# Kernel optimization log

Measured on AMD Instinct MI355X. Metric: run time of the kernel, lower is better.

## Reference

```python
import jax, jax.numpy as jnp
import numpy as np
from jax import lax

N, C, H, W = 32, 256, 32, 32
E, K, MLP = 8, 2, 4
CAP = 1.25
HID = MLP * C
LN_EPS = 1e-6


def setup_inputs() -> dict:
    key = jax.random.key(0)
    ks = jax.random.split(key, 12)
    s = 0.02
    return {
        "input": jax.random.normal(ks[0], (N, C, H, W), jnp.float32),
        "dw_kernel": jax.random.normal(ks[1], (C, 1, 7, 7), jnp.float32) * s,
        "dw_bias": jnp.zeros((C,), jnp.float32),
        "ln_gamma": jnp.ones((C,), jnp.float32),
        "ln_beta": jnp.zeros((C,), jnp.float32),
        "router_w": jax.random.normal(ks[2], (C, E), jnp.float32) * s,
        "w1": jax.random.normal(ks[3], (E, C, HID), jnp.float32) * s,
        "b1": jnp.zeros((E, HID), jnp.float32),
        "w2": jax.random.normal(ks[4], (E, HID, C), jnp.float32) * s,
        "b2": jnp.zeros((E, C), jnp.float32),
        "layer_scale": jnp.full((C, 1, 1), 1e-6, jnp.float32),
    }


def reference(input, dw_kernel, dw_bias, ln_gamma, ln_beta, router_w,
              w1, b1, w2, b2, layer_scale):
    # depthwise 7x7 conv (groups = C), NCHW
    x = lax.conv_general_dilated(
        input, dw_kernel, window_strides=(1, 1), padding=[(3, 3), (3, 3)],
        dimension_numbers=("NCHW", "OIHW", "NCHW"), feature_group_count=C)
    x = x + dw_bias[None, :, None, None]
    x = jnp.transpose(x, (0, 2, 3, 1))  # NHWC
    # LayerNorm over channels
    mu = jnp.mean(x, axis=-1, keepdims=True)
    var = jnp.mean(jnp.square(x - mu), axis=-1, keepdims=True)
    x = (x - mu) * lax.rsqrt(var + LN_EPS) * ln_gamma + ln_beta

    T = N * H * W
    x_flat = x.reshape(T, C)

    # router (eval mode of NoisyTopKRouter: no noise)
    logits = x_flat @ router_w                      # [T, E]
    top_logits, topi = lax.top_k(logits, K)          # [T, K]
    weights = jax.nn.softmax(top_logits, axis=-1)    # [T, K]
    priority = weights[:, 0]
    order = jnp.argsort(-priority)                   # descending priority

    # build K*T candidates, stably sorted by expert id
    token_idx = jnp.tile(order, K)                           # order.repeat(K)
    expert_id = topi[order].T.reshape(-1)
    gate_w = weights[order].T.reshape(-1)
    perm = jnp.argsort(expert_id)                            # stable
    token_idx, expert_id, gate_w = token_idx[perm], expert_id[perm], gate_w[perm]

    # capacity truncation
    Be = int(K * T * CAP / E + 0.5)
    counts = jnp.bincount(expert_id, length=E)
    starts = jnp.cumsum(counts) - counts
    pos = jnp.arange(K * T) - starts[expert_id]
    keep = pos < Be
    slot = jnp.where(keep, expert_id * Be + pos, E * Be)     # dump slot for drops

    # dispatch to capacity buffers [E, Be, C]
    buf = jnp.zeros((E * Be + 1, C), x_flat.dtype).at[slot].set(x_flat[token_idx])
    buf = buf[:E * Be].reshape(E, Be, C)

    # grouped expert MLP: Linear -> GELU(exact) -> Linear
    h = jax.nn.gelu(jnp.einsum("ebc,ech->ebh", buf, w1) + b1[:, None, :],
                    approximate=False)
    y = jnp.einsum("ebh,ehc->ebc", h, w2) + b2[:, None, :]

    # combine: gather back, gate-scale (zero for dropped), scatter-add
    y_pad = jnp.concatenate([y.reshape(E * Be, C),
                             jnp.zeros((1, C), y.dtype)], axis=0)
    contrib = y_pad[slot] * (gate_w * keep.astype(gate_w.dtype))[:, None]
    out = jnp.zeros((T, C), x_flat.dtype).at[token_idx].add(contrib)

    out = out.reshape(N, H, W, C).transpose(0, 3, 1, 2)      # NCHW
    # stochastic_depth_prob = 0 -> identity
    return input + layer_scale[None] * out
```

## Files before the change

kernel.cpp:

```cpp
#include <hip/hip_runtime.h>
#include <math.h>

#define TOK 32768
#define CH  256
#define HIDN 1024
#define NE  8
#define BE  10240
#define CNT_STRIDE 64

typedef __attribute__((ext_vector_type(8))) short bf16x8;
typedef __attribute__((ext_vector_type(4))) float f32x4;
typedef __attribute__((ext_vector_type(2))) long long2v;

__device__ __forceinline__ unsigned short f2bf(float f) {
    unsigned u = __builtin_bit_cast(unsigned, f);
    unsigned r = 0x7FFFu + ((u >> 16) & 1u);
    return (unsigned short)((u + r) >> 16);
}
__device__ __forceinline__ float bf2f(unsigned short u) {
    return __builtin_bit_cast(float, (unsigned)u << 16);
}
__device__ __forceinline__ unsigned pk8_lo(float a, float b, unsigned old) {
    return (unsigned)__builtin_amdgcn_cvt_pk_fp8_f32(a, b, (int)old, false);
}
__device__ __forceinline__ unsigned pk8_hi(float a, float b, unsigned old) {
    return (unsigned)__builtin_amdgcn_cvt_pk_fp8_f32(a, b, (int)old, true);
}
__device__ __forceinline__ f32x4 mfma8(long a, long b, f32x4 c) {
    return __builtin_amdgcn_mfma_f32_16x16x32_fp8_fp8(a, b, c, 0, 0, 0);
}

typedef __attribute__((address_space(3))) void lds_t;
typedef const __attribute__((address_space(1))) void gm_t;
#define GL16(gp, lp) __builtin_amdgcn_global_load_lds((gm_t*)(gp), (lds_t*)(lp), 16, 0, 0)

__global__ void k_init(int* cnt) { cnt[threadIdx.x] = 0; }

__global__ __launch_bounds__(256) void k_conv(const float* __restrict__ in,
                                              const float* __restrict__ kern,
                                              const float* __restrict__ bias,
                                              unsigned char* __restrict__ xc8) {
    __shared__ float img[1024];
    __shared__ float kwl[49];
    int t = threadIdx.x;
    int bid = blockIdx.x;
    int c = bid & 255;

    GL16(in + (size_t)bid * 1024 + t * 4, (char*)img + t * 16);
    if (t < 49) kwl[t] = kern[c * 49 + t];
    __syncthreads();

    int x0 = (t & 7) * 4, y = t >> 3;
    float b0 = bias[c];
    float acc[4] = {b0, b0, b0, b0};
#pragma unroll
    for (int jr = 0; jr < 7; ++jr) {
        int yy = y + jr - 3;
        if ((unsigned)yy < 32u) {
            float row[10];
#pragma unroll
            for (int k = 0; k < 10; ++k) {
                int xx = x0 - 3 + k;
                row[k] = ((unsigned)xx < 32u) ? img[yy * 32 + xx] : 0.f;
            }
#pragma unroll
            for (int kx = 0; kx < 7; ++kx) {
                float kv = kwl[jr * 7 + kx];
#pragma unroll
                for (int o = 0; o < 4; ++o) acc[o] = fmaf(row[o + kx], kv, acc[o]);
            }
        }
    }
    unsigned u = pk8_lo(acc[0], acc[1], 0u);
    u = pk8_hi(acc[2], acc[3], u);
    *(unsigned*)(xc8 + (size_t)bid * 1024 + y * 32 + x0) = u;
}

__global__ __launch_bounds__(512) void k_lnr(const unsigned char* __restrict__ xc8,
                                             const float* __restrict__ gamma,
                                             const float* __restrict__ beta,
                                             const float* __restrict__ rw,
                                             unsigned* __restrict__ xf8,
                                             int* __restrict__ e01,
                                             float2* __restrict__ gates) {
    __shared__ float acc[32][260];
    int t = threadIdx.x;
    int n = blockIdx.x >> 5, y = blockIdx.x & 31;
    int x4 = t & 7, ch = t >> 3;

#pragma unroll
    for (int i = 0; i < 4; ++i) {
        int c = i * 64 + ch;
        unsigned word = *(const unsigned*)(xc8 + ((size_t)(n * 256 + c)) * 1024 + y * 32 + x4 * 4);
        acc[x4 * 4 + 0][c] = __builtin_amdgcn_cvt_f32_fp8((int)word, 0);
        acc[x4 * 4 + 1][c] = __builtin_amdgcn_cvt_f32_fp8((int)word, 1);
        acc[x4 * 4 + 2][c] = __builtin_amdgcn_cvt_f32_fp8((int)word, 2);
        acc[x4 * 4 + 3][c] = __builtin_amdgcn_cvt_f32_fp8((int)word, 3);
    }
    __syncthreads();

    int lane = t & 63, w = t >> 6;
    float4 g4 = ((const float4*)gamma)[lane];
    float4 b4 = ((const float4*)beta)[lane];
    int c0 = lane * 4;
    float4 rwv[8];
#pragma unroll
    for (int j = 0; j < 4; ++j) {
        rwv[j * 2]     = *(const float4*)(rw + (size_t)(c0 + j) * 8);
        rwv[j * 2 + 1] = *(const float4*)(rw + (size_t)(c0 + j) * 8 + 4);
    }

#pragma unroll
    for (int k = 0; k < 4; ++k) {
        int tl = w * 4 + k;
        float4 v = *(const float4*)&acc[tl][lane * 4];
        float s = v.x + v.y + v.z + v.w;
        float q = v.x * v.x + v.y * v.y + v.z * v.z + v.w * v.w;
#pragma unroll
        for (int m = 1; m < 64; m <<= 1) { s += __shfl_xor(s, m); q += __shfl_xor(q, m); }
        float mean = s * (1.0f / 256.0f);
        float var  = q * (1.0f / 256.0f) - mean * mean;
        float rstd = rsqrtf(var + 1e-6f);

        float xn[4];
        xn[0] = (v.x - mean) * rstd * g4.x + b4.x;
        xn[1] = (v.y - mean) * rstd * g4.y + b4.y;
        xn[2] = (v.z - mean) * rstd * g4.z + b4.z;
        xn[3] = (v.w - mean) * rstd * g4.w + b4.w;

        unsigned px = pk8_lo(xn[0], xn[1], 0u);
        px = pk8_hi(xn[2], xn[3], px);
        int tok = n * 1024 + y * 32 + tl;
        xf8[tok * 64 + lane] = px;

        float p[8];
#pragma unroll
        for (int e = 0; e < 8; ++e) p[e] = 0.f;
#pragma unroll
        for (int j = 0; j < 4; ++j) {
            float xv = xn[j];
            const float* r0 = (const float*)&rwv[j * 2];
#pragma unroll
            for (int e = 0; e < 8; ++e) p[e] += xv * r0[e];
        }
#pragma unroll
        for (int m = 1; m < 64; m <<= 1) {
#pragma unroll
            for (int e = 0; e < 8; ++e) p[e] += __shfl_xor(p[e], m);
        }
        if (lane == 0) {
            int e0 = 0; float l0 = p[0];
#pragma unroll
            for (int e = 1; e < 8; ++e) if (p[e] > l0) { l0 = p[e]; e0 = e; }
            int e1 = -1; float l1 = -3.4e38f;
#pragma unroll
            for (int e = 0; e < 8; ++e) if (e != e0 && p[e] > l1) { l1 = p[e]; e1 = e; }
            float tt = expf(l1 - l0);
            float w0 = 1.0f / (1.0f + tt);
            e01[tok] = e0 | (e1 << 8);
            gates[tok] = make_float2(w0, 1.0f - w0);
        }
    }
}

__global__ __launch_bounds__(256) void k_assign(const int* __restrict__ e01,
                                                int* __restrict__ cnt,
                                                int* __restrict__ row_token,
                                                int2* __restrict__ slots) {
    __shared__ int lcnt[8];
    __shared__ int base[8];
    int t = threadIdx.x;
    if (t < 8) lcnt[t] = 0;
    __syncthreads();
    int tok = blockIdx.x * 256 + t;
    int ee = e01[tok];
    int e0 = ee & 255, e1 = (ee >> 8) & 255;
    int lp0 = atomicAdd(&lcnt[e0], 1);
    int lp1 = atomicAdd(&lcnt[e1], 1);
    __syncthreads();
    if (t < 8) base[t] = atomicAdd(cnt + t * CNT_STRIDE, lcnt[t]);
    __syncthreads();
    int pos0 = base[e0] + lp0;
    int pos1 = base[e1] + lp1;
    int slot0 = (pos0 < BE) ? e0 * BE + pos0 : -1;
    int slot1 = (pos1 < BE) ? e1 * BE + pos1 : -1;
    if (slot0 >= 0) row_token[slot0] = tok;
    if (slot1 >= 0) row_token[slot1] = tok;
    slots[tok] = make_int2(slot0, slot1);
}

__global__ __launch_bounds__(256) void k_pack_w1(const float* __restrict__ w1,
                                                 unsigned char* __restrict__ w1p) {
    int s = blockIdx.x * 256 + threadIdx.x;
    int l = s & 63, tile = s >> 6;
    int kp = tile & 3, h = (tile >> 2) & 1, hc = (tile >> 3) & 31, e = tile >> 8;
    int l15 = l & 15, l4 = l >> 4;
    int hid = hc * 32 + h * 16 + l15;
    int ch0 = kp * 64 + l4 * 8;
    const float* s0 = w1 + ((size_t)e * 256 + ch0) * 1024 + hid;
    float v[8], u[8];
#pragma unroll
    for (int b = 0; b < 8; ++b) { v[b] = s0[b * 1024]; u[b] = s0[(b + 32) * 1024]; }
    uint4 o;
    o.x = pk8_hi(v[2], v[3], pk8_lo(v[0], v[1], 0u));
    o.y = pk8_hi(v[6], v[7], pk8_lo(v[4], v[5], 0u));
    o.z = pk8_hi(u[2], u[3], pk8_lo(u[0], u[1], 0u));
    o.w = pk8_hi(u[6], u[7], pk8_lo(u[4], u[5], 0u));
    *(uint4*)(w1p + (size_t)tile * 1024 + l * 16) = o;
}

__global__ __launch_bounds__(256) void k_pack_w2(const float* __restrict__ w2,
                                                 unsigned char* __restrict__ w2p) {
    int s = blockIdx.x * 256 + threadIdx.x;
    int l = s & 63, tile = s >> 6;
    int np = tile & 7, hc = (tile >> 3) & 31, e = tile >> 8;
    int l15 = l & 15, l4 = l >> 4;
    float v[8], u[8];
#pragma unroll
    for (int b = 0; b < 8; ++b) {
        int hidl = ((b >> 2) & 1) * 16 + l4 * 4 + (b & 3);
        const float* s0 = w2 + ((size_t)e * 1024 + hc * 32 + hidl) * 256 + np * 32 + l15;
        v[b] = s0[0];
        u[b] = s0[16];
    }
    uint4 o;
    o.x = pk8_hi(v[2], v[3], pk8_lo(v[0], v[1], 0u));
    o.y = pk8_hi(v[6], v[7], pk8_lo(v[4], v[5], 0u));
    o.z = pk8_hi(u[2], u[3], pk8_lo(u[0], u[1], 0u));
    o.w = pk8_hi(u[6], u[7], pk8_lo(u[4], u[5], 0u));
    *(uint4*)(w2p + (size_t)tile * 1024 + l * 16) = o;
}

__global__ __launch_bounds__(256, 3) void k_mlp(const unsigned char* __restrict__ xf8,
                                                const unsigned char* __restrict__ w1p,
                                                const unsigned char* __restrict__ w2p,
                                                const float* __restrict__ b1,
                                                const float* __restrict__ b2,
                                                const int* __restrict__ cnt,
                                                const int* __restrict__ row_token,
                                                unsigned short* __restrict__ Y) {
    int bid = blockIdx.x;
    int e = bid & 7;
    int row0 = (bid >> 3) * 64;
    int nrows = min(cnt[e * CNT_STRIDE], BE);
    if (row0 >= nrows) return;

    __shared__ char smem[45056];
    char* const W1S0 = smem;
    char* const W1S1 = smem + 8192;
    char* const W2S0 = smem + 16384;
    char* const W2S1 = smem + 24576;
    char* const W2S2 = smem + 32768;
    char* const b1lds = smem + 40960;

    int t = threadIdx.x;
    int w = t >> 6, lane = t & 63;
    int l15 = lane & 15, l4 = lane >> 4;

    const unsigned char* w1e = w1p + (size_t)e * 262144;
    const unsigned char* w2e = w2p + (size_t)e * 262144;

    int ri = row0 + w * 16 + l15;
    int tok0 = (ri < nrows) ? row_token[e * BE + ri] : 0;
    long xr[8];
#pragma unroll
    for (int ks = 0; ks < 8; ++ks)
        xr[ks] = *(const long*)(xf8 + (size_t)tok0 * 256 + ks * 32 + l4 * 8);

    GL16((const char*)(b1 + e * HIDN) + t * 16, b1lds + t * 16);
    GL16(w1e + t * 16, W1S0 + t * 16);
    GL16(w1e + 4096 + t * 16, W1S0 + 4096 + t * 16);
    GL16(w2e + t * 16, W2S0 + t * 16);
    GL16(w2e + 4096 + t * 16, W2S0 + 4096 + t * 16);
    __builtin_amdgcn_sched_barrier(0);
    asm volatile("s_waitcnt vmcnt(2)" ::: "memory");
    __builtin_amdgcn_s_barrier();
    __builtin_amdgcn_sched_barrier(0);

    f32x4 yacc[16];
#pragma unroll
    for (int nc = 0; nc < 16; ++nc) yacc[nc] = f32x4{0.f, 0.f, 0.f, 0.f};

    long hfA = 0, hfB = 0;

    auto STEP = [&](const char* w1c, const char* w2r, char* w1f_, char* w2f_,
                    const unsigned char* g1, const unsigned char* g2,
                    bool doStage, bool doB, long hin, long& hout,
                    int b1off, bool last) {
        if (doStage) {
            GL16(g1 + t * 16, w1f_ + t * 16);
            GL16(g1 + 4096 + t * 16, w1f_ + 4096 + t * 16);
            GL16(g2 + t * 16, w2f_ + t * 16);
            GL16(g2 + 4096 + t * 16, w2f_ + 4096 + t * 16);
        }
        long w1fr[2][8];
#pragma unroll
        for (int h = 0; h < 2; ++h)
#pragma unroll
            for (int kp = 0; kp < 4; ++kp) {
                long2v q = *(const long2v*)(w1c + (h * 4 + kp) * 1024 + lane * 16);
                w1fr[h][kp * 2] = q.x;
                w1fr[h][kp * 2 + 1] = q.y;
            }
        f32x4 ha0 = f32x4{0.f, 0.f, 0.f, 0.f};
        f32x4 ha1 = f32x4{0.f, 0.f, 0.f, 0.f};
#pragma unroll
        for (int ks = 0; ks < 8; ++ks) {
            ha0 = mfma8(w1fr[0][ks], xr[ks], ha0);
            ha1 = mfma8(w1fr[1][ks], xr[ks], ha1);
        }
        if (doB) {
#pragma unroll
            for (int np = 0; np < 8; ++np) {
                long2v q = *(const long2v*)(w2r + np * 1024 + lane * 16);
                yacc[np * 2]     = mfma8(q.x, hin, yacc[np * 2]);
                yacc[np * 2 + 1] = mfma8(q.y, hin, yacc[np * 2 + 1]);
            }
        }
        float4 bv0 = *(const float4*)(b1lds + b1off + l4 * 16);
        float4 bv1 = *(const float4*)(b1lds + b1off + 64 + l4 * 16);
        float g[4];
#pragma unroll
        for (int j = 0; j < 4; ++j) {
            float vv = ha0[j] + ((const float*)&bv0)[j];
            g[j] = vv * __builtin_amdgcn_rcpf(1.0f + __builtin_amdgcn_exp2f(-2.4554672f * vv));
        }
        unsigned p0 = pk8_hi(g[2], g[3], pk8_lo(g[0], g[1], 0u));
#pragma unroll
        for (int j = 0; j < 4; ++j) {
            float vv = ha1[j] + ((const float*)&bv1)[j];
            g[j] = vv * __builtin_amdgcn_rcpf(1.0f + __builtin_amdgcn_exp2f(-2.4554672f * vv));
        }
        unsigned p1 = pk8_hi(g[2], g[3], pk8_lo(g[0], g[1], 0u));
        hout = (long)(((unsigned long)p1 << 32) | (unsigned long)p0);

        __builtin_amdgcn_sched_barrier(0);
        if (last) asm volatile("s_waitcnt vmcnt(0)" ::: "memory");
        else      asm volatile("s_waitcnt vmcnt(2)" ::: "memory");
        __builtin_amdgcn_s_barrier();
        __builtin_amdgcn_sched_barrier(0);
    };

    const char *w1r = W1S0, *w1f = W1S1;
    const char *w2red = W2S2, *w2cur = W2S0, *w2fil = W2S1;
    const unsigned char* g1 = w1e + 8192;
    const unsigned char* g2 = w2e + 8192;
    int b1off = 0;

#define ROTATE() { const char* _a = w1r; w1r = w1f; w1f = _a; \
                   const char* _b = w2red; w2red = w2cur; w2cur = w2fil; w2fil = _b; \
                   g1 += 8192; g2 += 8192; b1off += 128; }

    STEP(w1r, w2red, (char*)w1f, (char*)w2fil, g1, g2, true, false, hfB, hfA, b1off, false);
    ROTATE();
    for (int i = 0; i < 5; ++i) {
        STEP(w1r, w2red, (char*)w1f, (char*)w2fil, g1, g2, true, true, hfA, hfB, b1off, false); ROTATE();
        STEP(w1r, w2red, (char*)w1f, (char*)w2fil, g1, g2, true, true, hfB, hfA, b1off, false); ROTATE();
        STEP(w1r, w2red, (char*)w1f, (char*)w2fil, g1, g2, true, true, hfA, hfB, b1off, false); ROTATE();
        STEP(w1r, w2red, (char*)w1f, (char*)w2fil, g1, g2, true, true, hfB, hfA, b1off, false); ROTATE();
        STEP(w1r, w2red, (char*)w1f, (char*)w2fil, g1, g2, true, true, hfA, hfB, b1off, false); ROTATE();
        STEP(w1r, w2red, (char*)w1f, (char*)w2fil, g1, g2, true, true, hfB, hfA, b1off, false); ROTATE();
    }
    STEP(w1r, w2red, (char*)w1f, (char*)w2fil, g1, g2, false, true, hfA, hfB, b1off, true);
#pragma unroll
    for (int np = 0; np < 8; ++np) {
        long2v q = *(const long2v*)(w2cur + np * 1024 + lane * 16);
        yacc[np * 2]     = mfma8(q.x, hfB, yacc[np * 2]);
        yacc[np * 2 + 1] = mfma8(q.y, hfB, yacc[np * 2 + 1]);
    }
#undef ROTATE

#pragma unroll
    for (int nc = 0; nc < 16; ++nc) {
        float4 bv = *(const float4*)(b2 + e * 256 + nc * 16 + l4 * 4);
#pragma unroll
        for (int jj = 0; jj < 4; ++jj) yacc[nc][jj] += ((const float*)&bv)[jj];
    }
    __syncthreads();
    int lrow = w * 16 + l15;
#pragma unroll
    for (int nc = 0; nc < 16; ++nc) {
#pragma unroll
        for (int jp = 0; jp < 2; ++jp) {
            unsigned pk = (unsigned)f2bf(yacc[nc][jp * 2]) |
                          ((unsigned)f2bf(yacc[nc][jp * 2 + 1]) << 16);
            *(unsigned*)(smem + lrow * 520 + (nc * 16 + l4 * 4 + jp * 2) * 2) = pk;
        }
    }
    __syncthreads();
    {
        char* Yg = (char*)(Y + ((size_t)e * BE + row0) * 256);
#pragma unroll
        for (int i = 0; i < 8; ++i) {
            int flat = i * 4096 + t * 16;
            int row = flat >> 9, off = flat & 511;
            *(int4*)(Yg + row * 512 + off) = *(const int4*)(smem + row * 520 + off);
        }
    }
}

__global__ __launch_bounds__(256) void k_gather(const float* __restrict__ input,
                                                const unsigned short* __restrict__ Y,
                                                const int2* __restrict__ slots,
                                                const float2* __restrict__ gates,
                                                const float* __restrict__ ls,
                                                float* __restrict__ out) {
    __shared__ float acc[32][257];
    int t = threadIdx.x;
    int n = blockIdx.x >> 5, y = blockIdx.x & 31;

    {
        int tl = t & 31, chunk = t >> 5;
        int tok = n * 1024 + y * 32 + tl;
        int2  sl = slots[tok];
        float2 gw = gates[tok];
        int c0 = chunk * 32;
#pragma unroll
        for (int i = 0; i < 4; ++i) {
            int c = c0 + i * 8;
            float v[8];
#pragma unroll
            for (int k = 0; k < 8; ++k) v[k] = 0.f;
            if (sl.x >= 0) {
                bf16x8 yv = *(const bf16x8*)(Y + (size_t)sl.x * 256 + c);
#pragma unroll
                for (int k = 0; k < 8; ++k) v[k] += gw.x * bf2f((unsigned short)yv[k]);
            }
            if (sl.y >= 0) {
                bf16x8 yv = *(const bf16x8*)(Y + (size_t)sl.y * 256 + c);
#pragma unroll
                for (int k = 0; k < 8; ++k) v[k] += gw.y * bf2f((unsigned short)yv[k]);
            }
#pragma unroll
            for (int k = 0; k < 8; ++k) acc[tl][c + k] = v[k];
        }
    }
    __syncthreads();
    {
        int x = t & 31, c8 = t >> 5;
        size_t base = (size_t)n * 256 * 1024 + (size_t)y * 32 + x;
#pragma unroll
        for (int p = 0; p < 32; ++p) {
            int c = p * 8 + c8;
            size_t id = base + (size_t)c * 1024;
            out[id] = input[id] + ls[c] * acc[x][c];
        }
    }
}

extern "C" void kernel_launch(void* const* d_in, const int* in_sizes, int n_in,
                              void* d_out, int out_size, void* d_ws, size_t ws_size,
                              hipStream_t stream) {
    const float* input = (const float*)d_in[0];
    const float* dwk   = (const float*)d_in[1];
    const float* dwb   = (const float*)d_in[2];
    const float* gamma = (const float*)d_in[3];
    const float* beta  = (const float*)d_in[4];
    const float* rw    = (const float*)d_in[5];
    const float* w1    = (const float*)d_in[6];
    const float* b1    = (const float*)d_in[7];
    const float* w2    = (const float*)d_in[8];
    const float* b2    = (const float*)d_in[9];
    const float* ls    = (const float*)d_in[10];

    char* ws = (char*)d_ws;
    unsigned char*  xc8  = (unsigned char*)ws;
    unsigned short* Yb   = (unsigned short*)ws;
    unsigned*       xf8  = (unsigned*)(ws + 83886080);
    unsigned char*  w1p  = (unsigned char*)(ws + 100663296);
    unsigned char*  w2p  = (unsigned char*)(ws + 104857600);
    int*            rtok = (int*)(ws + 109051904);
    int2*           slots = (int2*)(ws + 109379584);
    float2*         gates = (float2*)(ws + 109641728);
    int*            e01  = (int*)(ws + 109903872);
    int*            cnt  = (int*)(ws + 110035968);

    k_init<<<1, NE * CNT_STRIDE, 0, stream>>>(cnt);
    k_conv<<<8192, 256, 0, stream>>>(input, dwk, dwb, xc8);
    k_lnr<<<1024, 512, 0, stream>>>(xc8, gamma, beta, rw, xf8, e01, gates);
    k_assign<<<128, 256, 0, stream>>>(e01, cnt, rtok, slots);
    k_pack_w1<<<512, 256, 0, stream>>>(w1, w1p);
    k_pack_w2<<<512, 256, 0, stream>>>(w2, w2p);
    k_mlp<<<1280, 256, 0, stream>>>((const unsigned char*)xf8, w1p, w2p, b1, b2, cnt, rtok, Yb);
    k_gather<<<1024, 256, 0, stream>>>(input, Yb, slots, gates, ls, (float*)d_out);
}
```

Baseline: 174.6 us.

## Switch expert MLP to 32x32x16 FP8 MFMA with 128-row tiles

The expert MLP kernel moves from 16x16x32 FP8 MFMA to 32x32x16 FP8 MFMA and doubles the rows per block from 64 to 128 tokens, halving the grid. The W1 and W2 packing is re-laid-out for the new operand fragment layout, and a new kernel pre-permutes the biases to match the accumulator layout. The aim is to raise MFMA throughput and reuse each staged weight tile across twice as many tokens, cutting weight traffic from L2 and LDS. In exchange each block uses more LDS and registers, occupancy drops to 2 blocks per CU, and fewer blocks may leave tail imbalance.

```diff
diff --git a/kernel.cpp b/kernel.cpp
--- a/kernel.cpp
+++ b/kernel.cpp
@@ -10,6 +10,7 @@
 
 typedef __attribute__((ext_vector_type(8))) short bf16x8;
 typedef __attribute__((ext_vector_type(4))) float f32x4;
+typedef __attribute__((ext_vector_type(16))) float f32x16;
 typedef __attribute__((ext_vector_type(2))) long long2v;
 
 __device__ __forceinline__ unsigned short f2bf(float f) {
@@ -26,8 +27,14 @@
 __device__ __forceinline__ unsigned pk8_hi(float a, float b, unsigned old) {
     return (unsigned)__builtin_amdgcn_cvt_pk_fp8_f32(a, b, (int)old, true);
 }
-__device__ __forceinline__ f32x4 mfma8(long a, long b, f32x4 c) {
-    return __builtin_amdgcn_mfma_f32_16x16x32_fp8_fp8(a, b, c, 0, 0, 0);
+__device__ __forceinline__ f32x16 mfma32(long a, long b, f32x16 c) {
+    return __builtin_amdgcn_mfma_f32_32x32x16_fp8_fp8(a, b, c, 0, 0, 0);
+}
+__device__ __forceinline__ f32x16 zero16() {
+    f32x16 z;
+#pragma unroll
+    for (int i = 0; i < 16; ++i) z[i] = 0.f;
+    return z;
 }
 
 typedef __attribute__((address_space(3))) void lds_t;
@@ -192,60 +199,73 @@
 __global__ __launch_bounds__(256) void k_pack_w1(const float* __restrict__ w1,
                                                  unsigned char* __restrict__ w1p) {
     int s = blockIdx.x * 256 + threadIdx.x;
-    int l = s & 63, tile = s >> 6;
-    int kp = tile & 3, h = (tile >> 2) & 1, hc = (tile >> 3) & 31, e = tile >> 8;
-    int l15 = l & 15, l4 = l >> 4;
-    int hid = hc * 32 + h * 16 + l15;
-    int ch0 = kp * 64 + l4 * 8;
-    const float* s0 = w1 + ((size_t)e * 256 + ch0) * 1024 + hid;
+    int l = s & 63, tp = s >> 6;
+    int kp = tp & 7, hc = (tp >> 3) & 31, e = tp >> 8;
+    int row = l & 31, h = l >> 5;
+    int hid = hc * 32 + row;
+    const float* s0 = w1 + ((size_t)e * 256 + kp * 32 + h * 8) * 1024 + hid;
     float v[8], u[8];
 #pragma unroll
-    for (int b = 0; b < 8; ++b) { v[b] = s0[b * 1024]; u[b] = s0[(b + 32) * 1024]; }
+    for (int b = 0; b < 8; ++b) { v[b] = s0[b * 1024]; u[b] = s0[(16 + b) * 1024]; }
     uint4 o;
     o.x = pk8_hi(v[2], v[3], pk8_lo(v[0], v[1], 0u));
     o.y = pk8_hi(v[6], v[7], pk8_lo(v[4], v[5], 0u));
     o.z = pk8_hi(u[2], u[3], pk8_lo(u[0], u[1], 0u));
     o.w = pk8_hi(u[6], u[7], pk8_lo(u[4], u[5], 0u));
-    *(uint4*)(w1p + (size_t)tile * 1024 + l * 16) = o;
+    *(uint4*)(w1p + (size_t)tp * 1024 + l * 16) = o;
 }
 
 __global__ __launch_bounds__(256) void k_pack_w2(const float* __restrict__ w2,
                                                  unsigned char* __restrict__ w2p) {
     int s = blockIdx.x * 256 + threadIdx.x;
-    int l = s & 63, tile = s >> 6;
-    int np = tile & 7, hc = (tile >> 3) & 31, e = tile >> 8;
-    int l15 = l & 15, l4 = l >> 4;
+    int l = s & 63, tp = s >> 6;
+    int ot = tp & 7, hc = (tp >> 3) & 31, e = tp >> 8;
+    int out = ot * 32 + (l & 31), h = l >> 5;
     float v[8], u[8];
 #pragma unroll
     for (int b = 0; b < 8; ++b) {
-        int hidl = ((b >> 2) & 1) * 16 + l4 * 4 + (b & 3);
-        const float* s0 = w2 + ((size_t)e * 1024 + hc * 32 + hidl) * 256 + np * 32 + l15;
-        v[b] = s0[0];
-        u[b] = s0[16];
+        int hid = hc * 32 + (b & 3) + 8 * (b >> 2) + 4 * h;
+        v[b] = w2[((size_t)e * 1024 + hid) * 256 + out];
+        u[b] = w2[((size_t)e * 1024 + hid + 16) * 256 + out];
     }
     uint4 o;
     o.x = pk8_hi(v[2], v[3], pk8_lo(v[0], v[1], 0u));
     o.y = pk8_hi(v[6], v[7], pk8_lo(v[4], v[5], 0u));
     o.z = pk8_hi(u[2], u[3], pk8_lo(u[0], u[1], 0u));
     o.w = pk8_hi(u[6], u[7], pk8_lo(u[4], u[5], 0u));
-    *(uint4*)(w2p + (size_t)tile * 1024 + l * 16) = o;
-}
-
-__global__ __launch_bounds__(256, 3) void k_mlp(const unsigned char* __restrict__ xf8,
+    *(uint4*)(w2p + (size_t)tp * 1024 + l * 16) = o;
+}
+
+__global__ __launch_bounds__(256) void k_pack_b(const float* __restrict__ b1,
+                                                const float* __restrict__ b2,
+                                                float* __restrict__ b1p,
+                                                float* __restrict__ b2p) {
+    int i = blockIdx.x * 256 + threadIdx.x;
+    if (i < 8192) {
+        int j = i & 15, h = (i >> 4) & 1, hc = (i >> 5) & 31, e = i >> 10;
+        b1p[i] = b1[e * 1024 + hc * 32 + (j & 3) + 8 * (j >> 2) + 4 * h];
+    } else if (i < 10240) {
+        int k = i - 8192;
+        int j = k & 15, ot = (k >> 4) & 7, h = (k >> 7) & 1, e = k >> 8;
+        b2p[k] = b2[e * 256 + ot * 32 + (j & 3) + 8 * (j >> 2) + 4 * h];
+    }
+}
+
+__global__ __launch_bounds__(256, 2) void k_mlp(const unsigned char* __restrict__ xf8,
                                                 const unsigned char* __restrict__ w1p,
                                                 const unsigned char* __restrict__ w2p,
-                                                const float* __restrict__ b1,
-                                                const float* __restrict__ b2,
+                                                const float* __restrict__ b1p,
+                                                const float* __restrict__ b2p,
                                                 const int* __restrict__ cnt,
                                                 const int* __restrict__ row_token,
                                                 unsigned short* __restrict__ Y) {
     int bid = blockIdx.x;
     int e = bid & 7;
-    int row0 = (bid >> 3) * 64;
+    int row0 = (bid >> 3) * 128;
     int nrows = min(cnt[e * CNT_STRIDE], BE);
     if (row0 >= nrows) return;
 
-    __shared__ char smem[45056];
+    __shared__ char smem[66560];
     char* const W1S0 = smem;
     char* const W1S1 = smem + 8192;
     char* const W2S0 = smem + 16384;
@@ -255,19 +275,19 @@
 
     int t = threadIdx.x;
     int w = t >> 6, lane = t & 63;
-    int l15 = lane & 15, l4 = lane >> 4;
+    int ltok = lane & 31, h = lane >> 5;
 
     const unsigned char* w1e = w1p + (size_t)e * 262144;
     const unsigned char* w2e = w2p + (size_t)e * 262144;
 
-    int ri = row0 + w * 16 + l15;
+    int ri = row0 + w * 32 + ltok;
     int tok0 = (ri < nrows) ? row_token[e * BE + ri] : 0;
-    long xr[8];
-#pragma unroll
-    for (int ks = 0; ks < 8; ++ks)
-        xr[ks] = *(const long*)(xf8 + (size_t)tok0 * 256 + ks * 32 + l4 * 8);
-
-    GL16((const char*)(b1 + e * HIDN) + t * 16, b1lds + t * 16);
+    long xr[16];
+#pragma unroll
+    for (int ks = 0; ks < 16; ++ks)
+        xr[ks] = *(const long*)(xf8 + (size_t)tok0 * 256 + ks * 16 + h * 8);
+
+    GL16((const char*)b1p + e * 4096 + t * 16, b1lds + t * 16);
     GL16(w1e + t * 16, W1S0 + t * 16);
     GL16(w1e + 4096 + t * 16, W1S0 + 4096 + t * 16);
     GL16(w2e + t * 16, W2S0 + t * 16);
@@ -277,62 +297,59 @@
     __builtin_amdgcn_s_barrier();
     __builtin_amdgcn_sched_barrier(0);
 
-    f32x4 yacc[16];
-#pragma unroll
-    for (int nc = 0; nc < 16; ++nc) yacc[nc] = f32x4{0.f, 0.f, 0.f, 0.f};
-
-    long hfA = 0, hfB = 0;
+    f32x16 yacc[8];
+#pragma unroll
+    for (int ot = 0; ot < 8; ++ot) yacc[ot] = zero16();
+
+    long hfA0 = 0, hfA1 = 0, hfB0 = 0, hfB1 = 0;
 
     auto STEP = [&](const char* w1c, const char* w2r, char* w1f_, char* w2f_,
                     const unsigned char* g1, const unsigned char* g2,
-                    bool doStage, bool doB, long hin, long& hout,
-                    int b1off, bool last) {
+                    bool doStage, bool doB, long hin0, long hin1,
+                    long& hout0, long& hout1, int b1off, bool last) {
         if (doStage) {
             GL16(g1 + t * 16, w1f_ + t * 16);
             GL16(g1 + 4096 + t * 16, w1f_ + 4096 + t * 16);
             GL16(g2 + t * 16, w2f_ + t * 16);
             GL16(g2 + 4096 + t * 16, w2f_ + 4096 + t * 16);
         }
-        long w1fr[2][8];
-#pragma unroll
-        for (int h = 0; h < 2; ++h)
-#pragma unroll
-            for (int kp = 0; kp < 4; ++kp) {
-                long2v q = *(const long2v*)(w1c + (h * 4 + kp) * 1024 + lane * 16);
-                w1fr[h][kp * 2] = q.x;
-                w1fr[h][kp * 2 + 1] = q.y;
+        long w1fr[16];
+#pragma unroll
+        for (int kp = 0; kp < 8; ++kp) {
+            long2v q = *(const long2v*)(w1c + kp * 1024 + lane * 16);
+            w1fr[kp * 2] = q.x;
+            w1fr[kp * 2 + 1] = q.y;
+        }
+        f32x16 ha = zero16();
+#pragma unroll
+        for (int ks = 0; ks < 16; ++ks) ha = mfma32(w1fr[ks], xr[ks], ha);
+        if (doB) {
+#pragma unroll
+            for (int ot = 0; ot < 8; ++ot) {
+                long2v q = *(const long2v*)(w2r + ot * 1024 + lane * 16);
+                yacc[ot] = mfma32(q.x, hin0, yacc[ot]);
+                yacc[ot] = mfma32(q.y, hin1, yacc[ot]);
             }
-        f32x4 ha0 = f32x4{0.f, 0.f, 0.f, 0.f};
-        f32x4 ha1 = f32x4{0.f, 0.f, 0.f, 0.f};
-#pragma unroll
-        for (int ks = 0; ks < 8; ++ks) {
-            ha0 = mfma8(w1fr[0][ks], xr[ks], ha0);
-            ha1 = mfma8(w1fr[1][ks], xr[ks], ha1);
-        }
-        if (doB) {
-#pragma unroll
-            for (int np = 0; np < 8; ++np) {
-                long2v q = *(const long2v*)(w2r + np * 1024 + lane * 16);
-                yacc[np * 2]     = mfma8(q.x, hin, yacc[np * 2]);
-                yacc[np * 2 + 1] = mfma8(q.y, hin, yacc[np * 2 + 1]);
-            }
-        }
-        float4 bv0 = *(const float4*)(b1lds + b1off + l4 * 16);
-        float4 bv1 = *(const float4*)(b1lds + b1off + 64 + l4 * 16);
-        float g[4];
-#pragma unroll
-        for (int j = 0; j < 4; ++j) {
-            float vv = ha0[j] + ((const float*)&bv0)[j];
+        }
+        float bb[16];
+#pragma unroll
+        for (int q = 0; q < 4; ++q) {
+            float4 bq = *(const float4*)(b1lds + b1off + h * 64 + q * 16);
+            bb[q * 4 + 0] = bq.x; bb[q * 4 + 1] = bq.y;
+            bb[q * 4 + 2] = bq.z; bb[q * 4 + 3] = bq.w;
+        }
+        float g[16];
+#pragma unroll
+        for (int j = 0; j < 16; ++j) {
+            float vv = ha[j] + bb[j];
             g[j] = vv * __builtin_amdgcn_rcpf(1.0f + __builtin_amdgcn_exp2f(-2.4554672f * vv));
         }
         unsigned p0 = pk8_hi(g[2], g[3], pk8_lo(g[0], g[1], 0u));
-#pragma unroll
-        for (int j = 0; j < 4; ++j) {
-            float vv = ha1[j] + ((const float*)&bv1)[j];
-            g[j] = vv * __builtin_amdgcn_rcpf(1.0f + __builtin_amdgcn_exp2f(-2.4554672f * vv));
-        }
-        unsigned p1 = pk8_hi(g[2], g[3], pk8_lo(g[0], g[1], 0u));
-        hout = (long)(((unsigned long)p1 << 32) | (unsigned long)p0);
+        unsigned p1 = pk8_hi(g[6], g[7], pk8_lo(g[4], g[5], 0u));
+        hout0 = (long)(((unsigned long)p1 << 32) | (unsigned long)p0);
+        unsigned p2 = pk8_hi(g[10], g[11], pk8_lo(g[8], g[9], 0u));
+        unsigned p3 = pk8_hi(g[14], g[15], pk8_lo(g[12], g[13], 0u));
+        hout1 = (long)(((unsigned long)p3 << 32) | (unsigned long)p2);
 
         __builtin_amdgcn_sched_barrier(0);
         if (last) asm volatile("s_waitcnt vmcnt(0)" ::: "memory");
@@ -351,47 +368,50 @@
                    const char* _b = w2red; w2red = w2cur; w2cur = w2fil; w2fil = _b; \
                    g1 += 8192; g2 += 8192; b1off += 128; }
 
-    STEP(w1r, w2red, (char*)w1f, (char*)w2fil, g1, g2, true, false, hfB, hfA, b1off, false);
+    STEP(w1r, w2red, (char*)w1f, (char*)w2fil, g1, g2, true, false, hfB0, hfB1, hfA0, hfA1, b1off, false);
     ROTATE();
     for (int i = 0; i < 5; ++i) {
-        STEP(w1r, w2red, (char*)w1f, (char*)w2fil, g1, g2, true, true, hfA, hfB, b1off, false); ROTATE();
-        STEP(w1r, w2red, (char*)w1f, (char*)w2fil, g1, g2, true, true, hfB, hfA, b1off, false); ROTATE();
-        STEP(w1r, w2red, (char*)w1f, (char*)w2fil, g1, g2, true, true, hfA, hfB, b1off, false); ROTATE();
-        STEP(w1r, w2red, (char*)w1f, (char*)w2fil, g1, g2, true, true, hfB, hfA, b1off, false); ROTATE();
-        STEP(w1r, w2red, (char*)w1f, (char*)w2fil, g1, g2, true, true, hfA, hfB, b1off, false); ROTATE();
-        STEP(w1r, w2red, (char*)w1f, (char*)w2fil, g1, g2, true, true, hfB, hfA, b1off, false); ROTATE();
-    }
-    STEP(w1r, w2red, (char*)w1f, (char*)w2fil, g1, g2, false, true, hfA, hfB, b1off, true);
-#pragma unroll
-    for (int np = 0; np < 8; ++np) {
-        long2v q = *(const long2v*)(w2cur + np * 1024 + lane * 16);
-        yacc[np * 2]     = mfma8(q.x, hfB, yacc[np * 2]);
-        yacc[np * 2 + 1] = mfma8(q.y, hfB, yacc[np * 2 + 1]);
+        STEP(w1r, w2red, (char*)w1f, (char*)w2fil, g1, g2, true, true, hfA0, hfA1, hfB0, hfB1, b1off, false); ROTATE();
+        STEP(w1r, w2red, (char*)w1f, (char*)w2fil, g1, g2, true, true, hfB0, hfB1, hfA0, hfA1, b1off, false); ROTATE();
+        STEP(w1r, w2red, (char*)w1f, (char*)w2fil, g1, g2, true, true, hfA0, hfA1, hfB0, hfB1, b1off, false); ROTATE();
+        STEP(w1r, w2red, (char*)w1f, (char*)w2fil, g1, g2, true, true, hfB0, hfB1, hfA0, hfA1, b1off, false); ROTATE();
+        STEP(w1r, w2red, (char*)w1f, (char*)w2fil, g1, g2, true, true, hfA0, hfA1, hfB0, hfB1, b1off, false); ROTATE();
+        STEP(w1r, w2red, (char*)w1f, (char*)w2fil, g1, g2, true, true, hfB0, hfB1, hfA0, hfA1, b1off, false); ROTATE();
+    }
+    STEP(w1r, w2red, (char*)w1f, (char*)w2fil, g1, g2, false, true, hfA0, hfA1, hfB0, hfB1, b1off, true);
+#pragma unroll
+    for (int ot = 0; ot < 8; ++ot) {
+        long2v q = *(const long2v*)(w2cur + ot * 1024 + lane * 16);
+        yacc[ot] = mfma32(q.x, hfB0, yacc[ot]);
+        yacc[ot] = mfma32(q.y, hfB1, yacc[ot]);
     }
 #undef ROTATE
 
-#pragma unroll
-    for (int nc = 0; nc < 16; ++nc) {
-        float4 bv = *(const float4*)(b2 + e * 256 + nc * 16 + l4 * 4);
-#pragma unroll
-        for (int jj = 0; jj < 4; ++jj) yacc[nc][jj] += ((const float*)&bv)[jj];
-    }
-    __syncthreads();
-    int lrow = w * 16 + l15;
-#pragma unroll
-    for (int nc = 0; nc < 16; ++nc) {
-#pragma unroll
-        for (int jp = 0; jp < 2; ++jp) {
-            unsigned pk = (unsigned)f2bf(yacc[nc][jp * 2]) |
-                          ((unsigned)f2bf(yacc[nc][jp * 2 + 1]) << 16);
-            *(unsigned*)(smem + lrow * 520 + (nc * 16 + l4 * 4 + jp * 2) * 2) = pk;
+    __syncthreads();
+    int tokrow = w * 32 + ltok;
+#pragma unroll
+    for (int ot = 0; ot < 8; ++ot) {
+        float bb[16];
+#pragma unroll
+        for (int q = 0; q < 4; ++q) {
+            float4 bq = *(const float4*)(b2p + e * 256 + h * 128 + ot * 16 + q * 4);
+            bb[q * 4 + 0] = bq.x; bb[q * 4 + 1] = bq.y;
+            bb[q * 4 + 2] = bq.z; bb[q * 4 + 3] = bq.w;
+        }
+#pragma unroll
+        for (int jp = 0; jp < 8; ++jp) {
+            float a0 = yacc[ot][jp * 2] + bb[jp * 2];
+            float a1 = yacc[ot][jp * 2 + 1] + bb[jp * 2 + 1];
+            unsigned pk = (unsigned)f2bf(a0) | ((unsigned)f2bf(a1) << 16);
+            int out = ot * 32 + ((jp * 2) & 3) + 8 * ((jp * 2) >> 2) + 4 * h;
+            *(unsigned*)(smem + tokrow * 520 + out * 2) = pk;
         }
     }
     __syncthreads();
     {
         char* Yg = (char*)(Y + ((size_t)e * BE + row0) * 256);
 #pragma unroll
-        for (int i = 0; i < 8; ++i) {
+        for (int i = 0; i < 16; ++i) {
             int flat = i * 4096 + t * 16;
             int row = flat >> 9, off = flat & 511;
             *(int4*)(Yg + row * 512 + off) = *(const int4*)(smem + row * 520 + off);
@@ -474,6 +494,8 @@
     float2*         gates = (float2*)(ws + 109641728);
     int*            e01  = (int*)(ws + 109903872);
     int*            cnt  = (int*)(ws + 110035968);
+    float*          b1p  = (float*)(ws + 110100480);
+    float*          b2p  = (float*)(ws + 110133248);
 
     k_init<<<1, NE * CNT_STRIDE, 0, stream>>>(cnt);
     k_conv<<<8192, 256, 0, stream>>>(input, dwk, dwb, xc8);
@@ -481,6 +503,7 @@
     k_assign<<<128, 256, 0, stream>>>(e01, cnt, rtok, slots);
     k_pack_w1<<<512, 256, 0, stream>>>(w1, w1p);
     k_pack_w2<<<512, 256, 0, stream>>>(w2, w2p);
-    k_mlp<<<1280, 256, 0, stream>>>((const unsigned char*)xf8, w1p, w2p, b1, b2, cnt, rtok, Yb);
+    k_pack_b<<<40, 256, 0, stream>>>(b1, b2, b1p, b2p);
+    k_mlp<<<640, 256, 0, stream>>>((const unsigned char*)xf8, w1p, w2p, b1p, b2p, cnt, rtok, Yb);
     k_gather<<<1024, 256, 0, stream>>>(input, Yb, slots, gates, ls, (float*)d_out);
 }
```

Result: slower. 192.1 us (+10.0%).
